# Performance work log

Measured on AMD Instinct MI355X. Metric: run time of the kernel, lower is better.

## Reference

```python
import jax, jax.numpy as jnp
import numpy as np

TAU = 0.07
EPS = 1e-6
LN_EPS = 1e-5  # torch nn.LayerNorm default
NORM_EPS = 1e-12  # torch F.normalize default


def _l2norm(x):
    n = jnp.sqrt(jnp.sum(x * x, axis=-1, keepdims=True))
    return x / jnp.maximum(n, NORM_EPS)


def setup_inputs() -> dict:
    key = jax.random.key(0)
    k1, k2, k3, k4 = jax.random.split(key, 4)
    B, N, D, K = 16, 2048, 512, 8
    f_raw = jax.random.normal(k1, (B, N, D), dtype=jnp.float32)
    f_q = jax.random.normal(k2, (B, D), dtype=jnp.float32)
    gt_mask = jax.random.randint(k3, (B, N), 0, 2) > 0
    q_bg = jax.random.normal(k4, (K, D), dtype=jnp.float32) * 0.02
    alpha = jnp.float32(1.0)
    ln_w = jnp.ones((D,), dtype=jnp.float32)
    ln_b = jnp.zeros((D,), dtype=jnp.float32)
    return {"f_raw": f_raw, "f_q": f_q, "gt_mask": gt_mask,
            "q_bg": q_bg, "alpha": alpha, "ln_w": ln_w, "ln_b": ln_b}


def reference(f_raw, f_q, gt_mask, q_bg, alpha, ln_w, ln_b):
    B, N, D = f_raw.shape
    # background prototypes via cross-attention (K queries)
    attn = jax.nn.softmax(jnp.einsum('kd,bnd->bkn', q_bg, f_raw) / jnp.sqrt(jnp.float32(D)), axis=-1)
    p_bg = jnp.einsum('bkn,bnd->bkd', attn, f_raw)  # [B,K,D]
    # projection of each token onto each prototype, summed (einsum instead of (B,N,K,D) broadcast)
    numer = jnp.einsum('bnd,bkd->bnk', f_raw, p_bg)
    denom = jnp.sum(p_bg * p_bg, axis=-1) + EPS        # [B,K]
    coef = numer / denom[:, None, :]                   # [B,N,K]
    f_bg = jnp.einsum('bnk,bkd->bnd', coef, p_bg)      # [B,N,D]
    # foreground = LayerNorm(f_raw - alpha * f_bg)
    x = f_raw - alpha * f_bg
    mu = jnp.mean(x, axis=-1, keepdims=True)
    var = jnp.mean((x - mu) ** 2, axis=-1, keepdims=True)
    f_fg = (x - mu) / jnp.sqrt(var + LN_EPS) * ln_w + ln_b
    # semantic scores vs query embedding
    sim = jnp.sum(_l2norm(f_fg) * _l2norm(f_q)[:, None, :], axis=-1)
    s_sem = jax.nn.sigmoid(sim / TAU)
    # compactness: min cosine distance of each token to a prototype
    dot = jnp.einsum('bnd,bkd->bnk', _l2norm(f_raw), _l2norm(p_bg))
    loss_compact = jnp.mean(jnp.min(1.0 - dot, axis=-1))
    # orthogonality: off-diagonal gram of normalized f_bg ([B,N,N])
    p_n = _l2norm(f_bg)
    gram = jnp.einsum('bnd,bmd->bnm', p_n, p_n)
    eye = jnp.eye(N, dtype=gram.dtype)[None]
    loss_orth = jnp.mean((gram * (1.0 - eye)) ** 2)
    # alignment: -log of positive scores (masked mean)
    m = gt_mask.astype(s_sem.dtype)
    cnt = jnp.sum(m)
    neg_log = -jnp.log(jnp.maximum(s_sem, EPS))
    loss_align = jnp.where(cnt > 0, jnp.sum(neg_log * m) / jnp.maximum(cnt, 1.0), 0.0)
    return f_fg, f_bg, p_bg, s_sem, loss_compact, loss_orth, loss_align
```

## Files before the change

kernel.cpp:

```cpp
#include <hip/hip_runtime.h>
#include <math.h>

#define Bb 16
#define Nn 2048
#define Dd 512
#define Kk 8

constexpr float TAU = 0.07f;
constexpr float EPSc = 1e-6f;
constexpr float LN_EPS = 1e-5f;
constexpr float NORM_EPS = 1e-12f;
constexpr float SCALE = 0.04419417382415922f;

constexpr size_t OUT_FFG  = 0;
constexpr size_t OUT_FBG  = (size_t)Bb*Nn*Dd;
constexpr size_t OUT_PBG  = OUT_FBG + (size_t)Bb*Nn*Dd;
constexpr size_t OUT_SSEM = OUT_PBG + (size_t)Bb*Kk*Dd;
constexpr size_t OUT_LOSS = OUT_SSEM + (size_t)Bb*Nn;

constexpr int    NCH = 64;
constexpr size_t WS_PBPART = 0;
constexpr size_t WS_SUMW   = WS_PBPART + (size_t)Bb*NCH*Kk*Dd;
constexpr size_t WS_NF2    = WS_SUMW + (size_t)Bb*NCH*Kk;
constexpr size_t WS_SF     = WS_NF2 + (size_t)Bb*Nn;
constexpr size_t WS_M      = WS_SF + (size_t)Bb*Nn;
constexpr size_t WS_IDEN   = WS_M + Bb*64;
constexpr size_t WS_INP    = WS_IDEN + Bb*Kk;
constexpr size_t WS_P1     = WS_INP + Bb*Kk;
constexpr size_t WS_FQN    = WS_P1 + Bb*Kk;
constexpr size_t WS_CP     = WS_FQN + (size_t)Bb*Dd;
constexpr size_t WS_P5A    = WS_CP + (size_t)Bb*Nn*Kk;
constexpr size_t WS_P5B    = WS_P5A + 2048;
constexpr size_t WS_TRB    = WS_P5B + 2048;

__device__ __forceinline__ float dot4(float4 a, float4 b) {
    return a.x*b.x + a.y*b.y + a.z*b.z + a.w*b.w;
}

using f32x4 = __attribute__((ext_vector_type(4))) float;
__device__ __forceinline__ void nt_store4(float* p, float4 v) {
    f32x4 t; t.x = v.x; t.y = v.y; t.z = v.z; t.w = v.w;
    __builtin_nontemporal_store(t, (f32x4*)p);
}

__global__ __launch_bounds__(512, 4) void k1_scores(const float* __restrict__ f_raw,
                                                    const float* __restrict__ q_bg,
                                                    float* __restrict__ ws) {
    int b = blockIdx.x >> 6;
    int chunk = blockIdx.x & 63;
    int tok0 = chunk * 32;
    int tid = threadIdx.x, lane = tid & 63, wave = tid >> 6;
    __shared__ float qls[Kk*Dd];
    __shared__ float wlds[32][8];
    __shared__ float swsum[8][8];
    for (int e = tid; e < Kk*Dd; e += 512) qls[e] = q_bg[e];
    __syncthreads();
    int sub = lane >> 4, idx = lane & 15;
    int tokl = wave*4 + sub;
    const float* ftok = f_raw + ((size_t)b*Nn + tok0 + tokl)*Dd;

    float a[8] = {0,0,0,0,0,0,0,0};
    float nf2 = 0.f, sf = 0.f;
    #pragma unroll
    for (int cc = 0; cc < 8; ++cc) {
        int o = cc*64 + idx*4;
        float4 f4 = *(const float4*)(ftok + o);
        #pragma unroll
        for (int k = 0; k < 8; ++k) {
            float4 q4 = *(const float4*)&qls[k*Dd + o];
            a[k] += dot4(f4, q4);
        }
        nf2 += dot4(f4, f4);
        sf  += f4.x + f4.y + f4.z + f4.w;
    }
    #pragma unroll
    for (int m = 1; m <= 8; m <<= 1) {
        #pragma unroll
        for (int k = 0; k < 8; ++k) a[k] += __shfl_xor(a[k], m, 64);
        nf2 += __shfl_xor(nf2, m, 64);
        sf  += __shfl_xor(sf, m, 64);
    }
    float w8[8];
    #pragma unroll
    for (int k = 0; k < 8; ++k) w8[k] = expf(a[k]*SCALE);
    if (idx == 0) {
        size_t n = (size_t)b*Nn + tok0 + tokl;
        ws[WS_NF2 + n] = nf2;
        ws[WS_SF + n]  = sf;
        *(float4*)&wlds[tokl][0] = make_float4(w8[0],w8[1],w8[2],w8[3]);
        *(float4*)&wlds[tokl][4] = make_float4(w8[4],w8[5],w8[6],w8[7]);
    }
    float sw[8];
    #pragma unroll
    for (int k = 0; k < 8; ++k) sw[k] = (idx == 0) ? w8[k] : 0.f;
    #pragma unroll
    for (int k = 0; k < 8; ++k) {
        sw[k] += __shfl_xor(sw[k], 16, 64);
        sw[k] += __shfl_xor(sw[k], 32, 64);
    }
    if (lane == 0) {
        *(float4*)&swsum[wave][0] = make_float4(sw[0],sw[1],sw[2],sw[3]);
        *(float4*)&swsum[wave][4] = make_float4(sw[4],sw[5],sw[6],sw[7]);
    }
    __syncthreads();
    if (tid < 8) {
        float s = 0.f;
        #pragma unroll
        for (int w = 0; w < 8; ++w) s += swsum[w][tid];
        ws[WS_SUMW + (size_t)(b*NCH + chunk)*8 + tid] = s;
    }
    int d = tid;
    const float* fcol = f_raw + ((size_t)b*Nn + tok0)*Dd + d;
    float acc[8] = {0,0,0,0,0,0,0,0};
    #pragma unroll 4
    for (int nn = 0; nn < 32; ++nn) {
        float f = fcol[(size_t)nn*Dd];
        float4 wa = *(const float4*)&wlds[nn][0];
        float4 wb = *(const float4*)&wlds[nn][4];
        acc[0]+=wa.x*f; acc[1]+=wa.y*f; acc[2]+=wa.z*f; acc[3]+=wa.w*f;
        acc[4]+=wb.x*f; acc[5]+=wb.y*f; acc[6]+=wb.z*f; acc[7]+=wb.w*f;
    }
    #pragma unroll
    for (int k = 0; k < 8; ++k)
        ws[WS_PBPART + ((size_t)(b*NCH + chunk)*8 + k)*Dd + d] = acc[k];
}

__global__ __launch_bounds__(256) void k3b1_reduce(float* __restrict__ ws,
                                                   float* __restrict__ out_pbg) {
    int b = blockIdx.x, k = blockIdx.y;
    int tid = threadIdx.x;
    float v = ws[WS_SUMW + (size_t)(b*NCH + (tid & 63))*8 + k];
    #pragma unroll
    for (int off = 32; off >= 1; off >>= 1) v += __shfl_xor(v, off, 64);
    float swt = 1.f / v;
    float s0 = 0.f, s1 = 0.f;
    #pragma unroll 4
    for (int ns = 0; ns < NCH; ++ns) {
        const float* p = ws + WS_PBPART + ((size_t)(b*NCH + ns)*8 + k)*Dd;
        s0 += p[tid];
        s1 += p[tid + 256];
    }
    out_pbg[(size_t)b*Kk*Dd + (size_t)k*Dd + tid]       = s0*swt;
    out_pbg[(size_t)b*Kk*Dd + (size_t)k*Dd + tid + 256] = s1*swt;
}

__global__ __launch_bounds__(256) void k3b2_stats(float* __restrict__ ws,
                                                  const float* __restrict__ pbg,
                                                  const float* __restrict__ f_q) {
    int b = blockIdx.x, tid = threadIdx.x;
    int lane = tid & 63, wave = tid >> 6;
    __shared__ float pb[Kk*Dd];
    __shared__ float mseg[64][4];
    __shared__ float p1seg[8][8];
    __shared__ float red[4];
    for (int e = tid; e < Kk*Dd; e += 256) pb[e] = pbg[(size_t)b*Kk*Dd + e];
    float q0 = f_q[b*Dd + tid], q1 = f_q[b*Dd + 256 + tid];
    float p2 = q0*q0 + q1*q1;
    #pragma unroll
    for (int off = 32; off >= 1; off >>= 1) p2 += __shfl_xor(p2, off, 64);
    if (lane == 0) red[wave] = p2;
    __syncthreads();
    float invq = 1.f/fmaxf(sqrtf(red[0]+red[1]+red[2]+red[3]), NORM_EPS);
    ws[WS_FQN + b*Dd + tid] = q0*invq;
    ws[WS_FQN + b*Dd + 256 + tid] = q1*invq;
    {
        int pair = tid >> 2, seg = tid & 3;
        int i = pair >> 3, j = pair & 7;
        float s = 0.f;
        for (int d = seg*128; d < seg*128 + 128; ++d) s += pb[i*Dd + d]*pb[j*Dd + d];
        mseg[pair][seg] = s;
    }
    if (tid < 64) {
        int k = tid >> 3, sg = tid & 7;
        float s1 = 0.f;
        for (int d = sg*64; d < sg*64 + 64; ++d) s1 += pb[k*Dd + d];
        p1seg[k][sg] = s1;
    }
    __syncthreads();
    if (tid < 64) {
        float m = mseg[tid][0] + mseg[tid][1] + mseg[tid][2] + mseg[tid][3];
        ws[WS_M + b*64 + tid] = m;
        if ((tid >> 3) == (tid & 7)) {
            int k = tid & 7;
            ws[WS_IDEN + b*Kk + k] = 1.f/(m + EPSc);
            ws[WS_INP + b*Kk + k] = 1.f/fmaxf(sqrtf(m), NORM_EPS);
        }
    }
    if (tid < 8) {
        float s1 = 0.f;
        #pragma unroll
        for (int sg = 0; sg < 8; ++sg) s1 += p1seg[tid][sg];
        ws[WS_P1 + b*Kk + tid] = s1;
    }
}

__global__ __launch_bounds__(512, 4) void k5_main(
    const float* __restrict__ f_raw, const int* __restrict__ gt_mask,
    const float* __restrict__ alpha_p, const float* __restrict__ ln_w,
    const float* __restrict__ ln_b, const float* __restrict__ pbg,
    float* __restrict__ ws, float* __restrict__ out_ffg,
    float* __restrict__ out_fbg, float* __restrict__ out_ssem)
{
    int b = blockIdx.x >> 6;
    int chunk = blockIdx.x & 63;
    int tok0 = chunk * 32;
    int tid = threadIdx.x, lane = tid & 63, wave = tid >> 6;
    __shared__ float pls[Kk*Dd];
    __shared__ float scl[32][12];
    __shared__ float Ml[64];
    __shared__ float idenl[8], inpl[8], p1l[8];
    __shared__ float al[8][4];
    for (int e = tid; e < Kk*Dd; e += 512) pls[e] = pbg[(size_t)b*Kk*Dd + e];
    if (tid >= 512-96 && tid < 512-32) Ml[tid-(512-96)] = ws[WS_M + b*64 + (tid-(512-96))];
    else if (tid >= 512-32 && tid < 512-8) {
        int g = (tid-(512-32)) >> 3, k = (tid-(512-32)) & 7;
        if      (g == 0) idenl[k] = ws[WS_IDEN + b*8 + k];
        else if (g == 1) inpl[k]  = ws[WS_INP  + b*8 + k];
        else             p1l[k]   = ws[WS_P1   + b*8 + k];
    }
    __syncthreads();
    int sub = lane >> 4, idx = lane & 15;
    int tokl = wave*4 + sub;
    const float* ftok = f_raw + ((size_t)b*Nn + tok0 + tokl)*Dd;

    float A[8] = {0,0,0,0,0,0,0,0};
    #pragma unroll
    for (int cc = 0; cc < 8; ++cc) {
        int o = cc*64 + idx*4;
        float4 f4 = *(const float4*)(ftok + o);
        #pragma unroll
        for (int k = 0; k < 8; ++k) {
            float4 p4 = *(const float4*)&pls[k*Dd + o];
            A[k] += dot4(f4, p4);
        }
    }
    #pragma unroll
    for (int m = 1; m <= 8; m <<= 1) {
        #pragma unroll
        for (int k = 0; k < 8; ++k) A[k] += __shfl_xor(A[k], m, 64);
    }
    float wcsum, wdsum;
    {
        size_t n = (size_t)b*Nn + tok0 + tokl;
        float nf2 = ws[WS_NF2 + n];
        float sf  = ws[WS_SF + n];
        float alpha = alpha_p[0];
        float coef[8], sca = 0.f, sp1 = 0.f;
        #pragma unroll
        for (int k = 0; k < 8; ++k) {
            coef[k] = A[k]*idenl[k];
            sca += coef[k]*A[k];
            sp1 += coef[k]*p1l[k];
        }
        float quad = 0.f;
        #pragma unroll
        for (int i = 0; i < 8; ++i) {
            float ti = 0.f;
            #pragma unroll
            for (int j = 0; j < 8; ++j) ti += Ml[i*8+j]*coef[j];
            quad += coef[i]*ti;
        }
        float sx  = sf - alpha*sp1;
        float sxx = nf2 - 2.f*alpha*sca + alpha*alpha*quad;
        float mu  = sx*(1.f/Dd);
        float var = sxx*(1.f/Dd) - mu*mu;
        float rstd = 1.f/sqrtf(fmaxf(var, 0.f) + LN_EPS);
        float invnf = 1.f/fmaxf(sqrtf(nf2), NORM_EPS);
        float cmin = 1e30f;
        #pragma unroll
        for (int k = 0; k < 8; ++k) cmin = fminf(cmin, 1.f - A[k]*invnf*inpl[k]);
        float invnb = 1.f/fmaxf(sqrtf(quad), NORM_EPS);
        float inb2 = invnb*invnb;
        float gnn = quad*inb2;
        float dloc = gnn*gnn;
        if (idx == 0) {
            *(float4*)&scl[tokl][0] = make_float4(coef[0],coef[1],coef[2],coef[3]);
            *(float4*)&scl[tokl][4] = make_float4(coef[4],coef[5],coef[6],coef[7]);
            *(float2*)&scl[tokl][8] = make_float2(mu, rstd);
            *(float4*)(ws + WS_CP + n*8)     = make_float4(coef[0]*invnb,coef[1]*invnb,coef[2]*invnb,coef[3]*invnb);
            *(float4*)(ws + WS_CP + n*8 + 4) = make_float4(coef[4]*invnb,coef[5]*invnb,coef[6]*invnb,coef[7]*invnb);
        }
        float cv = (idx == 0) ? cmin : 0.f;
        float dv = (idx == 0) ? dloc : 0.f;
        cv += __shfl_xor(cv, 16, 64); cv += __shfl_xor(cv, 32, 64);
        dv += __shfl_xor(dv, 16, 64); dv += __shfl_xor(dv, 32, 64);
        wcsum = cv; wdsum = dv;
    }
    float alpha = alpha_p[0];
    float ng2h[4], dqh[4];
    {
        int d0 = lane*4;
        float4 pbr[8];
        #pragma unroll
        for (int k = 0; k < 8; ++k) pbr[k] = *(const float4*)&pls[k*Dd + d0];
        float4 w4 = *(const float4*)(ln_w + d0);
        float4 b4 = *(const float4*)(ln_b + d0);
        float4 q4 = *(const float4*)(ws + WS_FQN + b*Dd + d0);
        #pragma unroll
        for (int t = 0; t < 4; ++t) {
            int lt = wave*4 + t;
            float4 cA = *(const float4*)&scl[lt][0];
            float4 cB = *(const float4*)&scl[lt][4];
            float2 mr = *(const float2*)&scl[lt][8];
            size_t rowoff = ((size_t)b*Nn + tok0 + lt)*Dd;
            float4 fv = *(const float4*)(f_raw + rowoff + d0);
            float4 fb;
            fb.x = cA.x*pbr[0].x + cA.y*pbr[1].x + cA.z*pbr[2].x + cA.w*pbr[3].x
                 + cB.x*pbr[4].x + cB.y*pbr[5].x + cB.z*pbr[6].x + cB.w*pbr[7].x;
            fb.y = cA.x*pbr[0].y + cA.y*pbr[1].y + cA.z*pbr[2].y + cA.w*pbr[3].y
                 + cB.x*pbr[4].y + cB.y*pbr[5].y + cB.z*pbr[6].y + cB.w*pbr[7].y;
            fb.z = cA.x*pbr[0].z + cA.y*pbr[1].z + cA.z*pbr[2].z + cA.w*pbr[3].z
                 + cB.x*pbr[4].z + cB.y*pbr[5].z + cB.z*pbr[6].z + cB.w*pbr[7].z;
            fb.w = cA.x*pbr[0].w + cA.y*pbr[1].w + cA.z*pbr[2].w + cA.w*pbr[3].w
                 + cB.x*pbr[4].w + cB.y*pbr[5].w + cB.z*pbr[6].w + cB.w*pbr[7].w;
            nt_store4(out_fbg + rowoff + d0, fb);
            float4 g;
            g.x = (fv.x - alpha*fb.x - mr.x)*mr.y*w4.x + b4.x;
            g.y = (fv.y - alpha*fb.y - mr.x)*mr.y*w4.y + b4.y;
            g.z = (fv.z - alpha*fb.z - mr.x)*mr.y*w4.z + b4.z;
            g.w = (fv.w - alpha*fb.w - mr.x)*mr.y*w4.w + b4.w;
            nt_store4(out_ffg + rowoff + d0, g);
            ng2h[t] = dot4(g, g);
            dqh[t]  = dot4(g, q4);
        }
    }
    float align_s = 0.f, align_c = 0.f;
    {
        int d0 = 256 + lane*4;
        float4 pbr[8];
        #pragma unroll
        for (int k = 0; k < 8; ++k) pbr[k] = *(const float4*)&pls[k*Dd + d0];
        float4 w4 = *(const float4*)(ln_w + d0);
        float4 b4 = *(const float4*)(ln_b + d0);
        float4 q4 = *(const float4*)(ws + WS_FQN + b*Dd + d0);
        #pragma unroll
        for (int t = 0; t < 4; ++t) {
            int lt = wave*4 + t;
            size_t n = (size_t)b*Nn + tok0 + lt;
            float4 cA = *(const float4*)&scl[lt][0];
            float4 cB = *(const float4*)&scl[lt][4];
            float2 mr = *(const float2*)&scl[lt][8];
            size_t rowoff = n*(size_t)Dd;
            float4 fv = *(const float4*)(f_raw + rowoff + d0);
            float4 fb;
            fb.x = cA.x*pbr[0].x + cA.y*pbr[1].x + cA.z*pbr[2].x + cA.w*pbr[3].x
                 + cB.x*pbr[4].x + cB.y*pbr[5].x + cB.z*pbr[6].x + cB.w*pbr[7].x;
            fb.y = cA.x*pbr[0].y + cA.y*pbr[1].y + cA.z*pbr[2].y + cA.w*pbr[3].y
                 + cB.x*pbr[4].y + cB.y*pbr[5].y + cB.z*pbr[6].y + cB.w*pbr[7].y;
            fb.z = cA.x*pbr[0].z + cA.y*pbr[1].z + cA.z*pbr[2].z + cA.w*pbr[3].z
                 + cB.x*pbr[4].z + cB.y*pbr[5].z + cB.z*pbr[6].z + cB.w*pbr[7].z;
            fb.w = cA.x*pbr[0].w + cA.y*pbr[1].w + cA.z*pbr[2].w + cA.w*pbr[3].w
                 + cB.x*pbr[4].w + cB.y*pbr[5].w + cB.z*pbr[6].w + cB.w*pbr[7].w;
            nt_store4(out_fbg + rowoff + d0, fb);
            float4 g;
            g.x = (fv.x - alpha*fb.x - mr.x)*mr.y*w4.x + b4.x;
            g.y = (fv.y - alpha*fb.y - mr.x)*mr.y*w4.y + b4.y;
            g.z = (fv.z - alpha*fb.z - mr.x)*mr.y*w4.z + b4.z;
            g.w = (fv.w - alpha*fb.w - mr.x)*mr.y*w4.w + b4.w;
            nt_store4(out_ffg + rowoff + d0, g);
            float ng2 = ng2h[t] + dot4(g, g);
            float dq  = dqh[t]  + dot4(g, q4);
            #pragma unroll
            for (int off = 32; off >= 1; off >>= 1) {
                ng2 += __shfl_xor(ng2, off, 64);
                dq  += __shfl_xor(dq,  off, 64);
            }
            float sim = dq * (1.f/fmaxf(sqrtf(ng2), NORM_EPS));
            float ssem = 1.f/(1.f + expf(-sim*(1.f/TAU)));
            if (lane == 0) {
                out_ssem[n] = ssem;
                if (gt_mask[n] != 0) { align_s += -logf(fmaxf(ssem, EPSc)); align_c += 1.f; }
            }
        }
    }
    if (lane == 0) {
        al[wave][0] = align_s; al[wave][1] = align_c;
        al[wave][2] = wcsum;   al[wave][3] = wdsum;
    }
    __syncthreads();
    if (tid == 0) {
        float as = 0.f, ac = 0.f, cs = 0.f, ds = 0.f;
        #pragma unroll
        for (int w = 0; w < 8; ++w) {
            as += al[w][0]; ac += al[w][1]; cs += al[w][2]; ds += al[w][3];
        }
        ws[WS_P5B + (size_t)blockIdx.x*2 + 0] = as;
        ws[WS_P5B + (size_t)blockIdx.x*2 + 1] = ac;
        ws[WS_P5A + (size_t)blockIdx.x*2 + 0] = cs;
        ws[WS_P5A + (size_t)blockIdx.x*2 + 1] = ds;
    }
}

__global__ __launch_bounds__(256) void k6s_gram(float* __restrict__ ws) {
    int b = blockIdx.x, tid = threadIdx.x;
    __shared__ float cps[256*8];
    __shared__ float Sred[4][64];
    __shared__ float Sfull[64];
    __shared__ float Alds[64];
    __shared__ float Mlds[64];
    int pr = tid & 63, g = tid >> 6;
    int i = pr >> 3, j = pr & 7;
    float s = 0.f;
    for (int tile = 0; tile < 8; ++tile) {
        __syncthreads();
        #pragma unroll
        for (int q = 0; q < 2; ++q)
            *(float4*)&cps[tid*8 + q*4] =
                *(const float4*)(ws + WS_CP + ((size_t)b*Nn + tile*256)*8 + tid*8 + q*4);
        __syncthreads();
        for (int nn = g*64; nn < g*64 + 64; ++nn)
            s += cps[nn*8 + i]*cps[nn*8 + j];
    }
    Sred[g][pr] = s;
    if (tid < 64) Mlds[tid] = ws[WS_M + b*64 + tid];
    __syncthreads();
    if (tid < 64) Sfull[tid] = Sred[0][tid]+Sred[1][tid]+Sred[2][tid]+Sred[3][tid];
    __syncthreads();
    if (tid < 64) {
        int ii = tid >> 3, jj = tid & 7;
        float a = 0.f;
        #pragma unroll
        for (int k = 0; k < 8; ++k) a += Mlds[ii*8+k]*Sfull[k*8+jj];
        Alds[tid] = a;
    }
    __syncthreads();
    if (tid < 64) {
        float p = Alds[tid]*Alds[(tid & 7)*8 + (tid >> 3)];
        #pragma unroll
        for (int off = 32; off >= 1; off >>= 1) p += __shfl_xor(p, off, 64);
        if (tid == 0) ws[WS_TRB + b] = p;
    }
}

__global__ __launch_bounds__(256) void k7_final(const float* __restrict__ ws,
                                                float* __restrict__ out_loss) {
    int tid = threadIdx.x, lane = tid & 63, wave = tid >> 6;
    __shared__ double red[4][4];
    double c = 0.0, dg = 0.0, as = 0.0, ac = 0.0;
    for (int idx = tid; idx < 1024; idx += 256) {
        c  += (double)ws[WS_P5A + idx*2 + 0];
        dg += (double)ws[WS_P5A + idx*2 + 1];
        as += (double)ws[WS_P5B + idx*2 + 0];
        ac += (double)ws[WS_P5B + idx*2 + 1];
    }
    #pragma unroll
    for (int off = 32; off >= 1; off >>= 1) {
        c  += __shfl_xor(c,  off, 64);
        dg += __shfl_xor(dg, off, 64);
        as += __shfl_xor(as, off, 64);
        ac += __shfl_xor(ac, off, 64);
    }
    if (lane == 0) { red[wave][0]=c; red[wave][1]=dg; red[wave][2]=as; red[wave][3]=ac; }
    __syncthreads();
    if (tid == 0) {
        double ct=0, dgt=0, ast=0, act=0, trt=0;
        for (int w = 0; w < 4; ++w) { ct+=red[w][0]; dgt+=red[w][1]; ast+=red[w][2]; act+=red[w][3]; }
        for (int b = 0; b < Bb; ++b) trt += (double)ws[WS_TRB + b];
        out_loss[0] = (float)(ct / (double)((size_t)Bb*Nn));
        out_loss[1] = (float)((trt - dgt) / ((double)Bb*(double)Nn*(double)Nn));
        out_loss[2] = (float)(act > 0.0 ? ast / (act > 1.0 ? act : 1.0) : 0.0);
    }
}

extern "C" void kernel_launch(void* const* d_in, const int* in_sizes, int n_in,
                              void* d_out, int out_size, void* d_ws, size_t ws_size,
                              hipStream_t stream) {
    (void)in_sizes; (void)n_in; (void)out_size; (void)ws_size;
    const float* f_raw   = (const float*)d_in[0];
    const float* f_q     = (const float*)d_in[1];
    const int*   gt_mask = (const int*)d_in[2];
    const float* q_bg    = (const float*)d_in[3];
    const float* alpha   = (const float*)d_in[4];
    const float* ln_w    = (const float*)d_in[5];
    const float* ln_b    = (const float*)d_in[6];
    float* out = (float*)d_out;
    float* ws  = (float*)d_ws;

    k1_scores<<<Bb*NCH, 512, 0, stream>>>(f_raw, q_bg, ws);
    k3b1_reduce<<<dim3(Bb, Kk), 256, 0, stream>>>(ws, out + OUT_PBG);
    k3b2_stats<<<Bb, 256, 0, stream>>>(ws, out + OUT_PBG, f_q);
    k5_main<<<Bb*NCH, 512, 0, stream>>>(f_raw, gt_mask, alpha, ln_w, ln_b,
                                        out + OUT_PBG, ws,
                                        out + OUT_FFG, out + OUT_FBG, out + OUT_SSEM);
    k6s_gram<<<Bb, 256, 0, stream>>>(ws);
    k7_final<<<1, 256, 0, stream>>>(ws, out + OUT_LOSS);
}
```

Before: 109.4 us.

## Fuse reduction and gram kernels, move token norm stats into main pass

Merges the two prototype-reduction kernels into one 1024-thread block per batch, and moves the per-token squared norm and sum computation from the score kernel into the main kernel, which removes a workspace round trip. Instead of writing per-token coefficient vectors and reducing them in a separate gram kernel, the main kernel now accumulates per-block 8x8 outer-product partial sums, and one final kernel reduces them together with the loss partials. The pipeline drops from six launches to four. The cost is extra shuffles and LDS traffic in the main kernel, and the prototype reduction now runs on only 16 blocks.

```diff
diff --git a/kernel.cpp b/kernel.cpp
--- a/kernel.cpp
+++ b/kernel.cpp
@@ -21,17 +21,14 @@
 constexpr int    NCH = 64;
 constexpr size_t WS_PBPART = 0;
 constexpr size_t WS_SUMW   = WS_PBPART + (size_t)Bb*NCH*Kk*Dd;
-constexpr size_t WS_NF2    = WS_SUMW + (size_t)Bb*NCH*Kk;
-constexpr size_t WS_SF     = WS_NF2 + (size_t)Bb*Nn;
-constexpr size_t WS_M      = WS_SF + (size_t)Bb*Nn;
+constexpr size_t WS_M      = WS_SUMW + (size_t)Bb*NCH*Kk;
 constexpr size_t WS_IDEN   = WS_M + Bb*64;
 constexpr size_t WS_INP    = WS_IDEN + Bb*Kk;
 constexpr size_t WS_P1     = WS_INP + Bb*Kk;
 constexpr size_t WS_FQN    = WS_P1 + Bb*Kk;
-constexpr size_t WS_CP     = WS_FQN + (size_t)Bb*Dd;
-constexpr size_t WS_P5A    = WS_CP + (size_t)Bb*Nn*Kk;
+constexpr size_t WS_SP     = WS_FQN + (size_t)Bb*Dd;
+constexpr size_t WS_P5A    = WS_SP + (size_t)Bb*NCH*64;
 constexpr size_t WS_P5B    = WS_P5A + 2048;
-constexpr size_t WS_TRB    = WS_P5B + 2048;
 
 __device__ __forceinline__ float dot4(float4 a, float4 b) {
     return a.x*b.x + a.y*b.y + a.z*b.z + a.w*b.w;
@@ -60,7 +57,6 @@
     const float* ftok = f_raw + ((size_t)b*Nn + tok0 + tokl)*Dd;
 
     float a[8] = {0,0,0,0,0,0,0,0};
-    float nf2 = 0.f, sf = 0.f;
     #pragma unroll
     for (int cc = 0; cc < 8; ++cc) {
         int o = cc*64 + idx*4;
@@ -70,23 +66,16 @@
             float4 q4 = *(const float4*)&qls[k*Dd + o];
             a[k] += dot4(f4, q4);
         }
-        nf2 += dot4(f4, f4);
-        sf  += f4.x + f4.y + f4.z + f4.w;
     }
     #pragma unroll
     for (int m = 1; m <= 8; m <<= 1) {
         #pragma unroll
         for (int k = 0; k < 8; ++k) a[k] += __shfl_xor(a[k], m, 64);
-        nf2 += __shfl_xor(nf2, m, 64);
-        sf  += __shfl_xor(sf, m, 64);
     }
     float w8[8];
     #pragma unroll
     for (int k = 0; k < 8; ++k) w8[k] = expf(a[k]*SCALE);
     if (idx == 0) {
-        size_t n = (size_t)b*Nn + tok0 + tokl;
-        ws[WS_NF2 + n] = nf2;
-        ws[WS_SF + n]  = sf;
         *(float4*)&wlds[tokl][0] = make_float4(w8[0],w8[1],w8[2],w8[3]);
         *(float4*)&wlds[tokl][4] = make_float4(w8[4],w8[5],w8[6],w8[7]);
     }
@@ -125,60 +114,77 @@
         ws[WS_PBPART + ((size_t)(b*NCH + chunk)*8 + k)*Dd + d] = acc[k];
 }
 
-__global__ __launch_bounds__(256) void k3b1_reduce(float* __restrict__ ws,
-                                                   float* __restrict__ out_pbg) {
-    int b = blockIdx.x, k = blockIdx.y;
-    int tid = threadIdx.x;
-    float v = ws[WS_SUMW + (size_t)(b*NCH + (tid & 63))*8 + k];
-    #pragma unroll
-    for (int off = 32; off >= 1; off >>= 1) v += __shfl_xor(v, off, 64);
-    float swt = 1.f / v;
-    float s0 = 0.f, s1 = 0.f;
-    #pragma unroll 4
-    for (int ns = 0; ns < NCH; ++ns) {
-        const float* p = ws + WS_PBPART + ((size_t)(b*NCH + ns)*8 + k)*Dd;
-        s0 += p[tid];
-        s1 += p[tid + 256];
-    }
-    out_pbg[(size_t)b*Kk*Dd + (size_t)k*Dd + tid]       = s0*swt;
-    out_pbg[(size_t)b*Kk*Dd + (size_t)k*Dd + tid + 256] = s1*swt;
-}
-
-__global__ __launch_bounds__(256) void k3b2_stats(float* __restrict__ ws,
-                                                  const float* __restrict__ pbg,
-                                                  const float* __restrict__ f_q) {
+__global__ __launch_bounds__(1024) void k3b_all(float* __restrict__ ws,
+                                                float* __restrict__ out_pbg,
+                                                const float* __restrict__ f_q) {
     int b = blockIdx.x, tid = threadIdx.x;
     int lane = tid & 63, wave = tid >> 6;
     __shared__ float pb[Kk*Dd];
-    __shared__ float mseg[64][4];
+    __shared__ float swt[8];
+    __shared__ float sumwseg[8][8];
+    __shared__ float redq[16];
+    __shared__ float mseg[64][8];
     __shared__ float p1seg[8][8];
-    __shared__ float red[4];
-    for (int e = tid; e < Kk*Dd; e += 256) pb[e] = pbg[(size_t)b*Kk*Dd + e];
-    float q0 = f_q[b*Dd + tid], q1 = f_q[b*Dd + 256 + tid];
-    float p2 = q0*q0 + q1*q1;
+    if (tid < 64) {
+        int k = tid & 7, sg = tid >> 3;
+        float s = 0.f;
+        #pragma unroll
+        for (int i = 0; i < 8; ++i)
+            s += ws[WS_SUMW + (size_t)(b*NCH + sg*8 + i)*8 + k];
+        sumwseg[sg][k] = s;
+    }
+    __syncthreads();
+    if (tid < 8) {
+        float s = 0.f;
+        #pragma unroll
+        for (int sg = 0; sg < 8; ++sg) s += sumwseg[sg][tid];
+        swt[tid] = 1.f/s;
+    }
+    float qv = (tid < 512) ? f_q[b*Dd + tid] : 0.f;
+    float p2 = qv*qv;
     #pragma unroll
     for (int off = 32; off >= 1; off >>= 1) p2 += __shfl_xor(p2, off, 64);
-    if (lane == 0) red[wave] = p2;
-    __syncthreads();
-    float invq = 1.f/fmaxf(sqrtf(red[0]+red[1]+red[2]+red[3]), NORM_EPS);
-    ws[WS_FQN + b*Dd + tid] = q0*invq;
-    ws[WS_FQN + b*Dd + 256 + tid] = q1*invq;
-    {
-        int pair = tid >> 2, seg = tid & 3;
+    if (lane == 0) redq[wave] = p2;
+    __syncthreads();
+    {
+        int e4 = tid*4;
+        float4 s4 = make_float4(0.f,0.f,0.f,0.f);
+        #pragma unroll 4
+        for (int ns = 0; ns < NCH; ++ns) {
+            float4 p = *(const float4*)(ws + WS_PBPART + (size_t)(b*NCH + ns)*(Kk*Dd) + e4);
+            s4.x += p.x; s4.y += p.y; s4.z += p.z; s4.w += p.w;
+        }
+        float sw = swt[e4 >> 9];
+        s4.x *= sw; s4.y *= sw; s4.z *= sw; s4.w *= sw;
+        *(float4*)&pb[e4] = s4;
+        *(float4*)(out_pbg + (size_t)b*Kk*Dd + e4) = s4;
+    }
+    if (tid < 512) {
+        float s = 0.f;
+        #pragma unroll
+        for (int w = 0; w < 16; ++w) s += redq[w];
+        float invq = 1.f/fmaxf(sqrtf(s), NORM_EPS);
+        ws[WS_FQN + (size_t)b*Dd + tid] = qv*invq;
+    }
+    __syncthreads();
+    if (tid < 512) {
+        int pair = tid >> 3, seg = tid & 7;
         int i = pair >> 3, j = pair & 7;
         float s = 0.f;
-        for (int d = seg*128; d < seg*128 + 128; ++d) s += pb[i*Dd + d]*pb[j*Dd + d];
+        for (int d = seg*64; d < seg*64 + 64; ++d) s += pb[i*Dd + d]*pb[j*Dd + d];
         mseg[pair][seg] = s;
-    }
+    } else if (tid < 576) {
+        int t2 = tid - 512;
+        int k = t2 >> 3, sg = t2 & 7;
+        float s = 0.f;
+        for (int d = sg*64; d < sg*64 + 64; ++d) s += pb[k*Dd + d];
+        p1seg[k][sg] = s;
+    }
+    __syncthreads();
     if (tid < 64) {
-        int k = tid >> 3, sg = tid & 7;
-        float s1 = 0.f;
-        for (int d = sg*64; d < sg*64 + 64; ++d) s1 += pb[k*Dd + d];
-        p1seg[k][sg] = s1;
-    }
-    __syncthreads();
-    if (tid < 64) {
-        float m = mseg[tid][0] + mseg[tid][1] + mseg[tid][2] + mseg[tid][3];
+        float m = 0.f;
+        #pragma unroll
+        for (int sg = 0; sg < 8; ++sg) m += mseg[tid][sg];
         ws[WS_M + b*64 + tid] = m;
         if ((tid >> 3) == (tid & 7)) {
             int k = tid & 7;
@@ -187,10 +193,10 @@
         }
     }
     if (tid < 8) {
-        float s1 = 0.f;
-        #pragma unroll
-        for (int sg = 0; sg < 8; ++sg) s1 += p1seg[tid][sg];
-        ws[WS_P1 + b*Kk + tid] = s1;
+        float s = 0.f;
+        #pragma unroll
+        for (int sg = 0; sg < 8; ++sg) s += p1seg[tid][sg];
+        ws[WS_P1 + b*Kk + tid] = s;
     }
 }
 
@@ -210,6 +216,7 @@
     __shared__ float Ml[64];
     __shared__ float idenl[8], inpl[8], p1l[8];
     __shared__ float al[8][4];
+    __shared__ float swp[8][64];
     for (int e = tid; e < Kk*Dd; e += 512) pls[e] = pbg[(size_t)b*Kk*Dd + e];
     if (tid >= 512-96 && tid < 512-32) Ml[tid-(512-96)] = ws[WS_M + b*64 + (tid-(512-96))];
     else if (tid >= 512-32 && tid < 512-8) {
@@ -224,6 +231,7 @@
     const float* ftok = f_raw + ((size_t)b*Nn + tok0 + tokl)*Dd;
 
     float A[8] = {0,0,0,0,0,0,0,0};
+    float nf2 = 0.f, sf = 0.f;
     #pragma unroll
     for (int cc = 0; cc < 8; ++cc) {
         int o = cc*64 + idx*4;
@@ -233,17 +241,18 @@
             float4 p4 = *(const float4*)&pls[k*Dd + o];
             A[k] += dot4(f4, p4);
         }
+        nf2 += dot4(f4, f4);
+        sf  += f4.x + f4.y + f4.z + f4.w;
     }
     #pragma unroll
     for (int m = 1; m <= 8; m <<= 1) {
         #pragma unroll
         for (int k = 0; k < 8; ++k) A[k] += __shfl_xor(A[k], m, 64);
+        nf2 += __shfl_xor(nf2, m, 64);
+        sf  += __shfl_xor(sf, m, 64);
     }
     float wcsum, wdsum;
     {
-        size_t n = (size_t)b*Nn + tok0 + tokl;
-        float nf2 = ws[WS_NF2 + n];
-        float sf  = ws[WS_SF + n];
         float alpha = alpha_p[0];
         float coef[8], sca = 0.f, sp1 = 0.f;
         #pragma unroll
@@ -273,13 +282,27 @@
         float inb2 = invnb*invnb;
         float gnn = quad*inb2;
         float dloc = gnn*gnn;
+        float cp[8];
+        #pragma unroll
+        for (int k = 0; k < 8; ++k) cp[k] = coef[k]*invnb;
         if (idx == 0) {
             *(float4*)&scl[tokl][0] = make_float4(coef[0],coef[1],coef[2],coef[3]);
             *(float4*)&scl[tokl][4] = make_float4(coef[4],coef[5],coef[6],coef[7]);
             *(float2*)&scl[tokl][8] = make_float2(mu, rstd);
-            *(float4*)(ws + WS_CP + n*8)     = make_float4(coef[0]*invnb,coef[1]*invnb,coef[2]*invnb,coef[3]*invnb);
-            *(float4*)(ws + WS_CP + n*8 + 4) = make_float4(coef[4]*invnb,coef[5]*invnb,coef[6]*invnb,coef[7]*invnb);
-        }
+        }
+        float spv[4];
+        #pragma unroll
+        for (int q = 0; q < 4; ++q) {
+            int e = idx*4 + q;
+            spv[q] = cp[e >> 3]*cp[e & 7];
+        }
+        #pragma unroll
+        for (int q = 0; q < 4; ++q) {
+            spv[q] += __shfl_xor(spv[q], 16, 64);
+            spv[q] += __shfl_xor(spv[q], 32, 64);
+        }
+        if (lane < 16)
+            *(float4*)&swp[wave][idx*4] = make_float4(spv[0],spv[1],spv[2],spv[3]);
         float cv = (idx == 0) ? cmin : 0.f;
         float dv = (idx == 0) ? dloc : 0.f;
         cv += __shfl_xor(cv, 16, 64); cv += __shfl_xor(cv, 32, 64);
@@ -378,6 +401,12 @@
         al[wave][2] = wcsum;   al[wave][3] = wdsum;
     }
     __syncthreads();
+    if (tid < 64) {
+        float s = 0.f;
+        #pragma unroll
+        for (int w = 0; w < 8; ++w) s += swp[w][tid];
+        ws[WS_SP + (size_t)blockIdx.x*64 + tid] = s;
+    }
     if (tid == 0) {
         float as = 0.f, ac = 0.f, cs = 0.f, ds = 0.f;
         #pragma unroll
@@ -391,58 +420,40 @@
     }
 }
 
-__global__ __launch_bounds__(256) void k6s_gram(float* __restrict__ ws) {
-    int b = blockIdx.x, tid = threadIdx.x;
-    __shared__ float cps[256*8];
-    __shared__ float Sred[4][64];
-    __shared__ float Sfull[64];
-    __shared__ float Alds[64];
-    __shared__ float Mlds[64];
-    int pr = tid & 63, g = tid >> 6;
-    int i = pr >> 3, j = pr & 7;
+__global__ __launch_bounds__(1024) void k8_final(const float* __restrict__ ws,
+                                                 float* __restrict__ out_loss) {
+    int tid = threadIdx.x, lane = tid & 63, wave = tid >> 6;
+    __shared__ float Sf[Bb][64];
+    __shared__ float Mf[Bb][64];
+    __shared__ float Af[Bb][64];
+    __shared__ float trb[Bb];
+    __shared__ double redd[16][4];
+    int b = tid >> 6, e = tid & 63;
     float s = 0.f;
-    for (int tile = 0; tile < 8; ++tile) {
-        __syncthreads();
-        #pragma unroll
-        for (int q = 0; q < 2; ++q)
-            *(float4*)&cps[tid*8 + q*4] =
-                *(const float4*)(ws + WS_CP + ((size_t)b*Nn + tile*256)*8 + tid*8 + q*4);
-        __syncthreads();
-        for (int nn = g*64; nn < g*64 + 64; ++nn)
-            s += cps[nn*8 + i]*cps[nn*8 + j];
-    }
-    Sred[g][pr] = s;
-    if (tid < 64) Mlds[tid] = ws[WS_M + b*64 + tid];
-    __syncthreads();
-    if (tid < 64) Sfull[tid] = Sred[0][tid]+Sred[1][tid]+Sred[2][tid]+Sred[3][tid];
-    __syncthreads();
-    if (tid < 64) {
-        int ii = tid >> 3, jj = tid & 7;
+    #pragma unroll 8
+    for (int c = 0; c < NCH; ++c)
+        s += ws[WS_SP + (size_t)(b*NCH + c)*64 + e];
+    Sf[b][e] = s;
+    Mf[b][e] = ws[WS_M + b*64 + e];
+    __syncthreads();
+    {
+        int ii = e >> 3, jj = e & 7;
         float a = 0.f;
         #pragma unroll
-        for (int k = 0; k < 8; ++k) a += Mlds[ii*8+k]*Sfull[k*8+jj];
-        Alds[tid] = a;
-    }
-    __syncthreads();
-    if (tid < 64) {
-        float p = Alds[tid]*Alds[(tid & 7)*8 + (tid >> 3)];
+        for (int k = 0; k < 8; ++k) a += Mf[b][ii*8+k]*Sf[b][k*8+jj];
+        Af[b][e] = a;
+    }
+    __syncthreads();
+    {
+        float p = Af[b][e]*Af[b][(e & 7)*8 + (e >> 3)];
         #pragma unroll
         for (int off = 32; off >= 1; off >>= 1) p += __shfl_xor(p, off, 64);
-        if (tid == 0) ws[WS_TRB + b] = p;
-    }
-}
-
-__global__ __launch_bounds__(256) void k7_final(const float* __restrict__ ws,
-                                                float* __restrict__ out_loss) {
-    int tid = threadIdx.x, lane = tid & 63, wave = tid >> 6;
-    __shared__ double red[4][4];
-    double c = 0.0, dg = 0.0, as = 0.0, ac = 0.0;
-    for (int idx = tid; idx < 1024; idx += 256) {
-        c  += (double)ws[WS_P5A + idx*2 + 0];
-        dg += (double)ws[WS_P5A + idx*2 + 1];
-        as += (double)ws[WS_P5B + idx*2 + 0];
-        ac += (double)ws[WS_P5B + idx*2 + 1];
-    }
+        if (lane == 0) trb[b] = p;
+    }
+    double c  = (double)ws[WS_P5A + (size_t)tid*2 + 0];
+    double dg = (double)ws[WS_P5A + (size_t)tid*2 + 1];
+    double as = (double)ws[WS_P5B + (size_t)tid*2 + 0];
+    double ac = (double)ws[WS_P5B + (size_t)tid*2 + 1];
     #pragma unroll
     for (int off = 32; off >= 1; off >>= 1) {
         c  += __shfl_xor(c,  off, 64);
@@ -450,12 +461,14 @@
         as += __shfl_xor(as, off, 64);
         ac += __shfl_xor(ac, off, 64);
     }
-    if (lane == 0) { red[wave][0]=c; red[wave][1]=dg; red[wave][2]=as; red[wave][3]=ac; }
+    if (lane == 0) { redd[wave][0]=c; redd[wave][1]=dg; redd[wave][2]=as; redd[wave][3]=ac; }
     __syncthreads();
     if (tid == 0) {
         double ct=0, dgt=0, ast=0, act=0, trt=0;
-        for (int w = 0; w < 4; ++w) { ct+=red[w][0]; dgt+=red[w][1]; ast+=red[w][2]; act+=red[w][3]; }
-        for (int b = 0; b < Bb; ++b) trt += (double)ws[WS_TRB + b];
+        for (int w = 0; w < 16; ++w) {
+            ct += redd[w][0]; dgt += redd[w][1]; ast += redd[w][2]; act += redd[w][3];
+        }
+        for (int bb = 0; bb < Bb; ++bb) trt += (double)trb[bb];
         out_loss[0] = (float)(ct / (double)((size_t)Bb*Nn));
         out_loss[1] = (float)((trt - dgt) / ((double)Bb*(double)Nn*(double)Nn));
         out_loss[2] = (float)(act > 0.0 ? ast / (act > 1.0 ? act : 1.0) : 0.0);
@@ -477,11 +490,9 @@
     float* ws  = (float*)d_ws;
 
     k1_scores<<<Bb*NCH, 512, 0, stream>>>(f_raw, q_bg, ws);
-    k3b1_reduce<<<dim3(Bb, Kk), 256, 0, stream>>>(ws, out + OUT_PBG);
-    k3b2_stats<<<Bb, 256, 0, stream>>>(ws, out + OUT_PBG, f_q);
+    k3b_all<<<Bb, 1024, 0, stream>>>(ws, out + OUT_PBG, f_q);
     k5_main<<<Bb*NCH, 512, 0, stream>>>(f_raw, gt_mask, alpha, ln_w, ln_b,
                                         out + OUT_PBG, ws,
                                         out + OUT_FFG, out + OUT_FBG, out + OUT_SSEM);
-    k6s_gram<<<Bb, 256, 0, stream>>>(ws);
-    k7_final<<<1, 256, 0, stream>>>(ws, out + OUT_LOSS);
-}
+    k8_final<<<1, 1024, 0, stream>>>(ws, out + OUT_LOSS);
+}
```

New measurement: 103.0 us, median of 3. 5.9% less time.
